# Optimization experiments

Measured on AMD Instinct MI355X. Metric: run time of the kernel, lower is better.

The kernel has to match this reference:

```python
import jax, jax.numpy as jnp
import numpy as np

DIM = 32  # fixed internal node dim
N_GRAPHS = 64


def setup_inputs() -> dict:
    key = jax.random.key(0)
    ks = jax.random.split(key, 16)
    N, E, F_N, F_E, H = 12500, 200000, 16, 8, 32
    inp = {
        "x": jax.random.normal(ks[0], (N, F_N), dtype=jnp.float32),
        "edge_index": jax.random.randint(ks[1], (2, E), 0, N, dtype=jnp.int64),
        "edge_attr": jax.random.normal(ks[2], (E, F_E), dtype=jnp.float32),
        "batch": jnp.sort(jax.random.randint(ks[3], (N,), 0, N_GRAPHS, dtype=jnp.int64)),
        "lin0_w": jax.random.normal(ks[4], (DIM, F_N), dtype=jnp.float32) * 0.1,
        "lin0_b": jax.random.normal(ks[5], (DIM,), dtype=jnp.float32) * 0.1,
        "nn_w": jax.random.normal(ks[6], (DIM * H, F_E), dtype=jnp.float32) * 0.1,
        "nn_b": jax.random.normal(ks[7], (DIM * H,), dtype=jnp.float32) * 0.1,
        "root_w": jax.random.normal(ks[8], (DIM, H), dtype=jnp.float32) * 0.1,
        "conv_b": jax.random.normal(ks[9], (H,), dtype=jnp.float32) * 0.1,
        "lin1_w": jax.random.normal(ks[10], (16, H), dtype=jnp.float32) * 0.1,
        "lin1_b": jax.random.normal(ks[11], (16,), dtype=jnp.float32) * 0.1,
        "lin2_w": jax.random.normal(ks[12], (1, 16), dtype=jnp.float32) * 0.1,
        "lin2_b": jax.random.normal(ks[13], (1,), dtype=jnp.float32) * 0.1,
    }
    return inp


def reference(x, edge_index, edge_attr, batch, lin0_w, lin0_b, nn_w, nn_b,
              root_w, conv_b, lin1_w, lin1_b, lin2_w, lin2_b):
    N = x.shape[0]
    H = conv_b.shape[0]
    # lin0 + relu -> node features [N, DIM]
    out = jax.nn.relu(x @ lin0_w.T + lin0_b)
    # NNConv: per-edge weight matrices from edge MLP (single Linear)
    src, dst = edge_index[0], edge_index[1]
    w_e = (edge_attr @ nn_w.T + nn_b).reshape(-1, DIM, H)  # [E, DIM, H]
    msg = jnp.einsum('ed,edh->eh', out[src], w_e)          # gather + per-edge matmul
    agg = jax.ops.segment_sum(msg, dst, num_segments=N)     # scatter-add
    h = jax.nn.relu(agg + out @ root_w + conv_b)             # root weight + bias
    # global add pool over graphs
    u = jax.ops.segment_sum(h, batch, num_segments=N_GRAPHS)  # [G, H]
    o = jax.nn.relu(u @ lin1_w.T + lin1_b)
    o = o @ lin2_w.T + lin2_b
    return o.reshape(-1)
```

## Files before the change

### kernel.cpp

```cpp
#include <hip/hip_runtime.h>

#define DIMN 32
#define HD   32
#define FN   16
#define FE   8
#define NG   64
#define CAP  64
#define K3T  512
#define K3W  (K3T / 64)

__global__ __launch_bounds__(256) void k1_out(
    const float* __restrict__ x, const float* __restrict__ lin0_w,
    const float* __restrict__ lin0_b,
    float* __restrict__ outn, float* __restrict__ aggfb, float* __restrict__ u,
    int* __restrict__ deg, int N)
{
    const int gt = blockIdx.x * 256 + threadIdx.x;
    if (gt >= N * DIMN) return;
    const int n = gt >> 5, d = gt & 31;

    float s = lin0_b[d];
    const float* xr = x + (size_t)n * FN;
    const float* wr = lin0_w + d * FN;
    #pragma unroll
    for (int j = 0; j < FN; ++j) s = fmaf(xr[j], wr[j], s);
    outn[gt] = fmaxf(s, 0.f);

    aggfb[gt] = 0.f;
    if (d == 0) deg[n] = 0;
    if (gt < NG * HD) u[gt] = 0.f;
}

__global__ __launch_bounds__(256) void kb_bucket(
    const int* __restrict__ ei, const float* __restrict__ ea,
    const float* __restrict__ outn, const float* __restrict__ nn_w,
    const float* __restrict__ nn_b,
    int* __restrict__ deg, int* __restrict__ esrc, float* __restrict__ eaB,
    float* __restrict__ aggfb, int E)
{
    const int e = blockIdx.x * 256 + threadIdx.x;
    if (e >= E) return;
    const int src = ei[e];
    const int dst = ei[E + e];
    const float4 w0 = *(const float4*)(ea + (size_t)e * FE);
    const float4 w1 = *(const float4*)(ea + (size_t)e * FE + 4);
    const int pos = atomicAdd(&deg[dst], 1);
    if (pos < CAP) {
        const size_t slot = (size_t)dst * CAP + pos;
        esrc[slot] = src;
        float4* eb = (float4*)(eaB + slot * 8);
        eb[0] = w0;
        eb[1] = w1;
    } else {
        const float ef[FE] = {w0.x, w0.y, w0.z, w0.w, w1.x, w1.y, w1.z, w1.w};
        for (int h = 0; h < HD; ++h) {
            float m = 0.f;
            for (int d = 0; d < DIMN; ++d) {
                float wdh = nn_b[d * HD + h];
                #pragma unroll
                for (int f = 0; f < FE; ++f)
                    wdh = fmaf(ef[f], nn_w[(d * HD + h) * FE + f], wdh);
                m = fmaf(outn[(size_t)src * DIMN + d], wdh, m);
            }
            atomicAdd(aggfb + (size_t)dst * HD + h, m);
        }
    }
}

#define EDGE_FMA(o, a) \
    S  = (S + (o));                      \
    T0 = fmaf((o), (a).x, T0);           \
    T1 = fmaf((o), (a).y, T1);           \
    T2 = fmaf((o), (a).z, T2);           \
    T3 = fmaf((o), (a).w, T3);

#define CONTRIB(DD, A) { \
    const int d_ = d0 + (DD); \
    const float4 ta_ = *(const float4*)&s_T[w * 256 + d_ * 8]; \
    const float4 tb_ = *(const float4*)&s_T[w * 256 + d_ * 8 + 4]; \
    const float2 so_ = s_SO[w * 32 + d_]; \
    const int b_ = d_ * 256 + h; \
    A = fmaf(ta_.x, s_nnw2[b_      ], A); \
    A = fmaf(ta_.y, s_nnw2[b_ +  32], A); \
    A = fmaf(ta_.z, s_nnw2[b_ +  64], A); \
    A = fmaf(ta_.w, s_nnw2[b_ +  96], A); \
    A = fmaf(tb_.x, s_nnw2[b_ + 128], A); \
    A = fmaf(tb_.y, s_nnw2[b_ + 160], A); \
    A = fmaf(tb_.z, s_nnw2[b_ + 192], A); \
    A = fmaf(tb_.w, s_nnw2[b_ + 224], A); \
    A = fmaf(so_.x, s_nnb[d_ * 32 + h], A); \
    A = fmaf(so_.y, s_rw [d_ * 32 + h], A); }

__global__ __launch_bounds__(K3T, 6) void k3_gather(
    const float* __restrict__ eaB, const float* __restrict__ outn,
    const int* __restrict__ esrc, const float* __restrict__ nn_w,
    const float* __restrict__ nn_b, const float* __restrict__ root_w,
    const float* __restrict__ conv_b, const int* __restrict__ deg,
    const float* __restrict__ aggfb, const int* __restrict__ batch,
    float* __restrict__ u, int N)
{
    __shared__ float  s_nnw2[DIMN * FE * HD];
    __shared__ float  s_nnb[DIMN * HD];
    __shared__ float  s_rw[DIMN * HD];
    __shared__ float  s_cb[HD];
    __shared__ float  s_T[K3W * 256];
    __shared__ float2 s_SO[K3W * 32];
    __shared__ float  s_V[K3W * 32];
    __shared__ int    s_G[K3W];

    const int tid = threadIdx.x;
    for (int i = tid; i < DIMN * FE * HD; i += K3T) {
        const int d = i >> 8, f = (i >> 5) & 7, hh = i & 31;
        s_nnw2[i] = nn_w[d * 256 + hh * 8 + f];
    }
    for (int i = tid; i < DIMN * HD; i += K3T) { s_nnb[i] = nn_b[i]; s_rw[i] = root_w[i]; }
    if (tid < HD) s_cb[tid] = conv_b[tid];
    __syncthreads();

    const int l = tid & 63;
    const int h = l & 31;
    const int p = l >> 5;
    const int w = tid >> 6;
    const int n = blockIdx.x * K3W + w;

    int gval = -1;
    if (n < N) {
        const int nu = __builtin_amdgcn_readfirstlane(n);
        const int dn = min(deg[nu], CAP);
        const int*   sp = esrc + (size_t)nu * CAP;
        const float* eb = eaB  + (size_t)nu * CAP * 8;
        const int f0 = 4 * p;

        float T0 = 0.f, T1 = 0.f, T2 = 0.f, T3 = 0.f, S = 0.f;

        const int jm = dn - 1;
        for (int j0 = 0; j0 < dn; j0 += 8) {
            const int j1 = min(j0 + 1, jm), j2 = min(j0 + 2, jm);
            const int j3 = min(j0 + 3, jm), j4 = min(j0 + 4, jm);
            const int j5 = min(j0 + 5, jm), j6 = min(j0 + 6, jm);
            const int j7 = min(j0 + 7, jm);

            const float4 a0 = *(const float4*)(eb + (size_t)j0 * 8 + f0);
            const float4 a1 = *(const float4*)(eb + (size_t)j1 * 8 + f0);
            const float4 a2 = *(const float4*)(eb + (size_t)j2 * 8 + f0);
            const float4 a3 = *(const float4*)(eb + (size_t)j3 * 8 + f0);
            const float4 a4 = *(const float4*)(eb + (size_t)j4 * 8 + f0);
            const float4 a5 = *(const float4*)(eb + (size_t)j5 * 8 + f0);
            const float4 a6 = *(const float4*)(eb + (size_t)j6 * 8 + f0);
            const float4 a7 = *(const float4*)(eb + (size_t)j7 * 8 + f0);

            const int s0 = sp[j0], s1 = sp[j1], s2 = sp[j2], s3 = sp[j3];
            const int s4 = sp[j4], s5 = sp[j5], s6 = sp[j6], s7 = sp[j7];
            float o0 = outn[(size_t)s0 * DIMN + h];
            float o1 = outn[(size_t)s1 * DIMN + h];
            float o2 = outn[(size_t)s2 * DIMN + h];
            float o3 = outn[(size_t)s3 * DIMN + h];
            float o4 = outn[(size_t)s4 * DIMN + h];
            float o5 = outn[(size_t)s5 * DIMN + h];
            float o6 = outn[(size_t)s6 * DIMN + h];
            float o7 = outn[(size_t)s7 * DIMN + h];

            o1 = (j0 + 1 <= jm) ? o1 : 0.f;
            o2 = (j0 + 2 <= jm) ? o2 : 0.f;
            o3 = (j0 + 3 <= jm) ? o3 : 0.f;
            o4 = (j0 + 4 <= jm) ? o4 : 0.f;
            o5 = (j0 + 5 <= jm) ? o5 : 0.f;
            o6 = (j0 + 6 <= jm) ? o6 : 0.f;
            o7 = (j0 + 7 <= jm) ? o7 : 0.f;

            EDGE_FMA(o0, a0) EDGE_FMA(o1, a1) EDGE_FMA(o2, a2) EDGE_FMA(o3, a3)
            EDGE_FMA(o4, a4) EDGE_FMA(o5, a5) EDGE_FMA(o6, a6) EDGE_FMA(o7, a7)
        }

        *(float4*)&s_T[w * 256 + h * 8 + f0] = make_float4(T0, T1, T2, T3);
        if (p == 0) s_SO[w * 32 + h] = make_float2(S, outn[(size_t)nu * DIMN + h]);

        const float base = aggfb[(size_t)nu * HD + h] + s_cb[h];

        float acc0 = 0.f, acc1 = 0.f, acc2 = 0.f, acc3 = 0.f;
        const int d0 = p << 4;
        #pragma unroll
        for (int dd = 0; dd < 16; dd += 4) {
            CONTRIB(dd + 0, acc0)
            CONTRIB(dd + 1, acc1)
            CONTRIB(dd + 2, acc2)
            CONTRIB(dd + 3, acc3)
        }
        float acc = (acc0 + acc1) + (acc2 + acc3);
        acc += __shfl_xor(acc, 32);

        const float v = fmaxf(acc + base, 0.f);
        if (p == 0) s_V[w * 32 + h] = v;
        gval = batch[nu];
    }
    if (l == 0) s_G[w] = gval;
    __syncthreads();

    if (tid < 32) {
        float accp = 0.f;
        int   gc   = -1;
        #pragma unroll
        for (int ww = 0; ww < K3W; ++ww) {
            const int gg = s_G[ww];
            if (gg >= 0) {
                const float vv = s_V[ww * 32 + tid];
                if (gg != gc) {
                    if (gc >= 0) atomicAdd(u + (size_t)gc * HD + tid, accp);
                    gc = gg;
                    accp = vv;
                } else {
                    accp += vv;
                }
            }
        }
        if (gc >= 0) atomicAdd(u + (size_t)gc * HD + tid, accp);
    }
}

__global__ __launch_bounds__(64) void k4_head(
    const float* __restrict__ u, const float* __restrict__ lin1_w,
    const float* __restrict__ lin1_b, const float* __restrict__ lin2_w,
    const float* __restrict__ lin2_b, float* __restrict__ outp)
{
    const int g = threadIdx.x;
    if (g >= NG) return;

    float ur[HD];
    #pragma unroll
    for (int hh = 0; hh < HD; ++hh) ur[hh] = u[(size_t)g * HD + hh];

    float acc = lin2_b[0];
    #pragma unroll
    for (int i = 0; i < 16; ++i) {
        float o = lin1_b[i];
        #pragma unroll
        for (int hh = 0; hh < HD; ++hh)
            o = fmaf(ur[hh], lin1_w[i * HD + hh], o);
        o = fmaxf(o, 0.f);
        acc = fmaf(o, lin2_w[i], acc);
    }
    outp[g] = acc;
}

extern "C" void kernel_launch(void* const* d_in, const int* in_sizes, int n_in,
                              void* d_out, int out_size, void* d_ws, size_t ws_size,
                              hipStream_t stream)
{
    const float* x      = (const float*)d_in[0];
    const int*   ei     = (const int*)  d_in[1];
    const float* ea     = (const float*)d_in[2];
    const int*   batch  = (const int*)  d_in[3];
    const float* lin0_w = (const float*)d_in[4];
    const float* lin0_b = (const float*)d_in[5];
    const float* nn_w   = (const float*)d_in[6];
    const float* nn_b   = (const float*)d_in[7];
    const float* root_w = (const float*)d_in[8];
    const float* conv_b = (const float*)d_in[9];
    const float* lin1_w = (const float*)d_in[10];
    const float* lin1_b = (const float*)d_in[11];
    const float* lin2_w = (const float*)d_in[12];
    const float* lin2_b = (const float*)d_in[13];

    const int N = in_sizes[0] / FN;
    const int E = in_sizes[2] / FE;

    float* ws    = (float*)d_ws;
    float* eaB   = ws;
    float* outn  = eaB  + (size_t)N * CAP * 8;
    float* aggfb = outn + (size_t)N * DIMN;
    float* u     = aggfb + (size_t)N * DIMN;
    int*   deg   = (int*)(u + (size_t)NG * HD);
    int*   esrc  = deg + N;

    const int nb1 = (N * DIMN + 255) / 256;
    k1_out<<<nb1, 256, 0, stream>>>(x, lin0_w, lin0_b, outn, aggfb, u, deg, N);

    const int nbb = (E + 255) / 256;
    kb_bucket<<<nbb, 256, 0, stream>>>(ei, ea, outn, nn_w, nn_b, deg, esrc, eaB,
                                       aggfb, E);

    const int nb3 = (N + K3W - 1) / K3W;
    k3_gather<<<nb3, K3T, 0, stream>>>(eaB, outn, esrc, nn_w, nn_b, root_w, conv_b,
                                       deg, aggfb, batch, u, N);

    k4_head<<<1, 64, 0, stream>>>(u, lin1_w, lin1_b, lin2_w, lin2_b, (float*)d_out);
}
```

Baseline: 158.9 us.

## Pre-gather source node features into per-destination buckets during bucketing

The bucketing kernel now runs 8 threads per edge and copies the source node's 32-float feature row into a per-destination bucket array, so the gather kernel reads contiguous data instead of chasing src indices. The gather loop is also split into a full 8-edge main loop and a single clamped tail. This removes dependent index loads and scattered reads from the gather kernel, at the cost of a much larger workspace write (N*64*32 floats) and 8x more threads in the bucketing pass.

Result: no change. 159.0 us (+0.0%).

```diff
diff --git a/kernel.cpp b/kernel.cpp
--- a/kernel.cpp
+++ b/kernel.cpp
@@ -35,24 +35,32 @@
     const int* __restrict__ ei, const float* __restrict__ ea,
     const float* __restrict__ outn, const float* __restrict__ nn_w,
     const float* __restrict__ nn_b,
-    int* __restrict__ deg, int* __restrict__ esrc, float* __restrict__ eaB,
+    int* __restrict__ deg, float* __restrict__ eaB, float* __restrict__ outB,
     float* __restrict__ aggfb, int E)
 {
-    const int e = blockIdx.x * 256 + threadIdx.x;
+    const int t = blockIdx.x * 256 + threadIdx.x;
+    const int e   = t >> 3;
+    const int sub = t & 7;
     if (e >= E) return;
     const int src = ei[e];
     const int dst = ei[E + e];
-    const float4 w0 = *(const float4*)(ea + (size_t)e * FE);
-    const float4 w1 = *(const float4*)(ea + (size_t)e * FE + 4);
-    const int pos = atomicAdd(&deg[dst], 1);
+
+    int pos = 0;
+    if (sub == 0) pos = atomicAdd(&deg[dst], 1);
+    pos = __shfl(pos, (threadIdx.x & 63) & ~7);
+
     if (pos < CAP) {
         const size_t slot = (size_t)dst * CAP + pos;
-        esrc[slot] = src;
-        float4* eb = (float4*)(eaB + slot * 8);
-        eb[0] = w0;
-        eb[1] = w1;
-    } else {
-        const float ef[FE] = {w0.x, w0.y, w0.z, w0.w, w1.x, w1.y, w1.z, w1.w};
+        const float4 q = *(const float4*)(outn + (size_t)src * DIMN + sub * 4);
+        *(float4*)(outB + slot * 32 + sub * 4) = q;
+        if (sub < 2) {
+            const float4 w = *(const float4*)(ea + (size_t)e * FE + sub * 4);
+            *(float4*)(eaB + slot * 8 + sub * 4) = w;
+        }
+    } else if (sub == 0) {
+        float ef[FE];
+        #pragma unroll
+        for (int f = 0; f < FE; ++f) ef[f] = ea[(size_t)e * FE + f];
         for (int h = 0; h < HD; ++h) {
             float m = 0.f;
             for (int d = 0; d < DIMN; ++d) {
@@ -92,8 +100,8 @@
     A = fmaf(so_.y, s_rw [d_ * 32 + h], A); }
 
 __global__ __launch_bounds__(K3T, 6) void k3_gather(
-    const float* __restrict__ eaB, const float* __restrict__ outn,
-    const int* __restrict__ esrc, const float* __restrict__ nn_w,
+    const float* __restrict__ eaB, const float* __restrict__ outB,
+    const float* __restrict__ outn, const float* __restrict__ nn_w,
     const float* __restrict__ nn_b, const float* __restrict__ root_w,
     const float* __restrict__ conv_b, const int* __restrict__ deg,
     const float* __restrict__ aggfb, const int* __restrict__ batch,
@@ -127,19 +135,39 @@
     if (n < N) {
         const int nu = __builtin_amdgcn_readfirstlane(n);
         const int dn = min(deg[nu], CAP);
-        const int*   sp = esrc + (size_t)nu * CAP;
+        const float* ob = outB + (size_t)nu * CAP * 32;
         const float* eb = eaB  + (size_t)nu * CAP * 8;
         const int f0 = 4 * p;
 
         float T0 = 0.f, T1 = 0.f, T2 = 0.f, T3 = 0.f, S = 0.f;
 
-        const int jm = dn - 1;
-        for (int j0 = 0; j0 < dn; j0 += 8) {
+        int j0 = 0;
+        for (; j0 + 8 <= dn; j0 += 8) {
+            const float4 a0 = *(const float4*)(eb + (size_t)(j0 + 0) * 8 + f0);
+            const float4 a1 = *(const float4*)(eb + (size_t)(j0 + 1) * 8 + f0);
+            const float4 a2 = *(const float4*)(eb + (size_t)(j0 + 2) * 8 + f0);
+            const float4 a3 = *(const float4*)(eb + (size_t)(j0 + 3) * 8 + f0);
+            const float4 a4 = *(const float4*)(eb + (size_t)(j0 + 4) * 8 + f0);
+            const float4 a5 = *(const float4*)(eb + (size_t)(j0 + 5) * 8 + f0);
+            const float4 a6 = *(const float4*)(eb + (size_t)(j0 + 6) * 8 + f0);
+            const float4 a7 = *(const float4*)(eb + (size_t)(j0 + 7) * 8 + f0);
+            const float o0 = ob[(size_t)(j0 + 0) * 32 + h];
+            const float o1 = ob[(size_t)(j0 + 1) * 32 + h];
+            const float o2 = ob[(size_t)(j0 + 2) * 32 + h];
+            const float o3 = ob[(size_t)(j0 + 3) * 32 + h];
+            const float o4 = ob[(size_t)(j0 + 4) * 32 + h];
+            const float o5 = ob[(size_t)(j0 + 5) * 32 + h];
+            const float o6 = ob[(size_t)(j0 + 6) * 32 + h];
+            const float o7 = ob[(size_t)(j0 + 7) * 32 + h];
+
+            EDGE_FMA(o0, a0) EDGE_FMA(o1, a1) EDGE_FMA(o2, a2) EDGE_FMA(o3, a3)
+            EDGE_FMA(o4, a4) EDGE_FMA(o5, a5) EDGE_FMA(o6, a6) EDGE_FMA(o7, a7)
+        }
+        if (j0 < dn) {
+            const int jm = dn - 1;
             const int j1 = min(j0 + 1, jm), j2 = min(j0 + 2, jm);
             const int j3 = min(j0 + 3, jm), j4 = min(j0 + 4, jm);
             const int j5 = min(j0 + 5, jm), j6 = min(j0 + 6, jm);
-            const int j7 = min(j0 + 7, jm);
-
             const float4 a0 = *(const float4*)(eb + (size_t)j0 * 8 + f0);
             const float4 a1 = *(const float4*)(eb + (size_t)j1 * 8 + f0);
             const float4 a2 = *(const float4*)(eb + (size_t)j2 * 8 + f0);
@@ -147,29 +175,21 @@
             const float4 a4 = *(const float4*)(eb + (size_t)j4 * 8 + f0);
             const float4 a5 = *(const float4*)(eb + (size_t)j5 * 8 + f0);
             const float4 a6 = *(const float4*)(eb + (size_t)j6 * 8 + f0);
-            const float4 a7 = *(const float4*)(eb + (size_t)j7 * 8 + f0);
-
-            const int s0 = sp[j0], s1 = sp[j1], s2 = sp[j2], s3 = sp[j3];
-            const int s4 = sp[j4], s5 = sp[j5], s6 = sp[j6], s7 = sp[j7];
-            float o0 = outn[(size_t)s0 * DIMN + h];
-            float o1 = outn[(size_t)s1 * DIMN + h];
-            float o2 = outn[(size_t)s2 * DIMN + h];
-            float o3 = outn[(size_t)s3 * DIMN + h];
-            float o4 = outn[(size_t)s4 * DIMN + h];
-            float o5 = outn[(size_t)s5 * DIMN + h];
-            float o6 = outn[(size_t)s6 * DIMN + h];
-            float o7 = outn[(size_t)s7 * DIMN + h];
-
+            const float o0 = ob[(size_t)j0 * 32 + h];
+            float o1 = ob[(size_t)j1 * 32 + h];
+            float o2 = ob[(size_t)j2 * 32 + h];
+            float o3 = ob[(size_t)j3 * 32 + h];
+            float o4 = ob[(size_t)j4 * 32 + h];
+            float o5 = ob[(size_t)j5 * 32 + h];
+            float o6 = ob[(size_t)j6 * 32 + h];
             o1 = (j0 + 1 <= jm) ? o1 : 0.f;
             o2 = (j0 + 2 <= jm) ? o2 : 0.f;
             o3 = (j0 + 3 <= jm) ? o3 : 0.f;
             o4 = (j0 + 4 <= jm) ? o4 : 0.f;
             o5 = (j0 + 5 <= jm) ? o5 : 0.f;
             o6 = (j0 + 6 <= jm) ? o6 : 0.f;
-            o7 = (j0 + 7 <= jm) ? o7 : 0.f;
-
             EDGE_FMA(o0, a0) EDGE_FMA(o1, a1) EDGE_FMA(o2, a2) EDGE_FMA(o3, a3)
-            EDGE_FMA(o4, a4) EDGE_FMA(o5, a5) EDGE_FMA(o6, a6) EDGE_FMA(o7, a7)
+            EDGE_FMA(o4, a4) EDGE_FMA(o5, a5) EDGE_FMA(o6, a6)
         }
 
         *(float4*)&s_T[w * 256 + h * 8 + f0] = make_float4(T0, T1, T2, T3);
@@ -265,22 +285,22 @@
     const int E = in_sizes[2] / FE;
 
     float* ws    = (float*)d_ws;
-    float* eaB   = ws;
+    float* outB  = ws;
+    float* eaB   = outB + (size_t)N * CAP * 32;
     float* outn  = eaB  + (size_t)N * CAP * 8;
     float* aggfb = outn + (size_t)N * DIMN;
     float* u     = aggfb + (size_t)N * DIMN;
     int*   deg   = (int*)(u + (size_t)NG * HD);
-    int*   esrc  = deg + N;
 
     const int nb1 = (N * DIMN + 255) / 256;
     k1_out<<<nb1, 256, 0, stream>>>(x, lin0_w, lin0_b, outn, aggfb, u, deg, N);
 
-    const int nbb = (E + 255) / 256;
-    kb_bucket<<<nbb, 256, 0, stream>>>(ei, ea, outn, nn_w, nn_b, deg, esrc, eaB,
+    const int nbb = ((size_t)E * 8 + 255) / 256;
+    kb_bucket<<<nbb, 256, 0, stream>>>(ei, ea, outn, nn_w, nn_b, deg, eaB, outB,
                                        aggfb, E);
 
     const int nb3 = (N + K3W - 1) / K3W;
-    k3_gather<<<nb3, K3T, 0, stream>>>(eaB, outn, esrc, nn_w, nn_b, root_w, conv_b,
+    k3_gather<<<nb3, K3T, 0, stream>>>(eaB, outB, outn, nn_w, nn_b, root_w, conv_b,
                                        deg, aggfb, batch, u, N);
 
     k4_head<<<1, 64, 0, stream>>>(u, lin1_w, lin1_b, lin2_w, lin2_b, (float*)d_out);
```
